# Kernel tuning notes

Measured on AMD Instinct MI355X. Metric: run time of the kernel, lower is better.

## Reference

```python
import jax, jax.numpy as jnp
import numpy as np

ALPHA = (0.02, 0.04, 0.08, 0.16)
CHAMFER_W, SMOOTH_W, CURVATURE_W = 1.0, 1.0, 0.3
NS = (8192, 4096, 2048, 1024)
B = 2


def _sqdist(a, b):
    # a: [B,N,3], b: [B,M,3] -> [B,N,M] squared euclidean distance
    return (jnp.sum(a * a, axis=-1)[:, :, None]
            - 2.0 * jnp.einsum('bnc,bmc->bnm', a, b)
            + jnp.sum(b * b, axis=-1)[:, None, :])


def _knn(d, k):
    # k smallest distances + indices along last axis
    neg, idx = jax.lax.top_k(-d, k)
    return -neg, idx


def _gather(points, idx):
    # points: [B,M,C], idx: [B,N,K] -> [B,N,K,C]
    return jax.vmap(lambda p, i: p[i])(points, idx)


def _scale_loss(pc1, pc2, flow):
    # pc1, pc2, flow: [B,3,N]-like -> permute to points-last layout
    p1 = jnp.transpose(pc1, (0, 2, 1))   # [B,N,3]
    p2 = jnp.transpose(pc2, (0, 2, 1))   # [B,M,3]
    fl = jnp.transpose(flow, (0, 2, 1))  # [B,N,3]
    warp = p1 + fl                        # warped pc1

    # curvature of pc2 (10-NN on pc2 itself)
    _, k22 = _knn(_sqdist(p2, p2), 10)
    cv2 = jnp.sum(_gather(p2, k22) - p2[:, :, None, :], axis=2) / 9.0  # [B,M,3]

    # 10-NN on pc1 (shared for warped curvature and smoothness; 9-NN is prefix)
    _, k11 = _knn(_sqdist(p1, p1), 10)
    cvw = jnp.sum(_gather(warp, k11) - warp[:, :, None, :], axis=2) / 9.0  # [B,N,3]

    k9 = k11[:, :, :9]
    gfl = _gather(fl, k9)  # [B,N,9,3]
    smooth = jnp.sum(jnp.linalg.norm(gfl - fl[:, :, None, :], axis=3), axis=2) / 8.0  # [B,N]

    # chamfer between warped pc1 and pc2
    d12 = _sqdist(warp, p2)               # [B,N,M]
    dist1 = jnp.min(d12, axis=-1)         # [B,N]
    dist2 = jnp.min(d12, axis=1)          # [B,M]

    # inverse-distance interpolation of pc2 curvature onto warped pc1 (5-NN)
    dist, kidx = _knn(d12, 5)             # [B,N,5]
    gcv = _gather(cv2, kidx)              # [B,N,5,3]
    w = 1.0 / (dist + 1e-8)
    w = w / jnp.sum(w, axis=2, keepdims=True)
    inter = jnp.sum(w[..., None] * gcv, axis=2)  # [B,N,3]

    chamfer = jnp.mean(jnp.sum(dist1, axis=1)) + jnp.mean(jnp.sum(dist2, axis=1))
    smoothness = jnp.mean(jnp.sum(smooth, axis=1))
    curv = jnp.mean(jnp.sum(jnp.sum((inter - cvw) ** 2, axis=2), axis=1))
    return chamfer, smoothness, curv


def setup_inputs() -> dict:
    key = jax.random.key(0)
    keys = jax.random.split(key, 12)
    out = {}
    names = ['pc1', 'pc2', 'flow']
    k = 0
    for name in names:
        for i, n in enumerate(NS):
            scale = 1.0 if name != 'flow' else 0.1
            out[f'{name}_{i}'] = scale * jax.random.normal(keys[k], (B, 3, n), dtype=jnp.float32)
            k += 1
    return out


def reference(pc1_0, pc1_1, pc1_2, pc1_3,
              pc2_0, pc2_1, pc2_2, pc2_3,
              flow_0, flow_1, flow_2, flow_3):
    pcs1 = (pc1_0, pc1_1, pc1_2, pc1_3)
    pcs2 = (pc2_0, pc2_1, pc2_2, pc2_3)
    flows = (flow_0, flow_1, flow_2, flow_3)
    ch = sm = cv = jnp.float32(0.0)
    for a, p1, p2, fl in zip(ALPHA, pcs1, pcs2, flows):
        c, s, k = _scale_loss(p1, p2, fl)
        ch = ch + a * c
        sm = sm + a * s
        cv = cv + a * k
    total = CHAMFER_W * ch + CURVATURE_W * cv + SMOOTH_W * sm
    return jnp.reshape(total, (1,))
```

## Files before the change

### kernel.cpp

```cpp
#include <hip/hip_runtime.h>
#include <math.h>


#define BLOCK 512
#define UNIT 1024
#define NTOT 15360
#define MASKC 0xFFFFE000u
#define PB 340

typedef unsigned int uint;

struct Params {
  const float* pc1[4];
  const float* pc2[4];
  const float* fl[4];
  float4* cv2;
  float4* cvw;
  float* out;
};

__device__ __forceinline__ void decode(int r, int wv, int& s, int& b,
                                       int& i0, int& lo, int& N, int& cpw,
                                       int& off, float& alpha) {
  int rr;
  if (r < 256)      { s = 0; rr = r; }
  else if (r < 320) { s = 1; rr = r - 256; }
  else if (r < 336) { s = 2; rr = r - 320; }
  else              { s = 3; rr = r - 336; }
  N = 8192 >> s;
  cpw = 8 >> s;
  int perb = 128 >> (2 * s);
  b = rr >> (7 - 2 * s);
  int chunk = rr & (perb - 1);
  int qg = (chunk << s) + (wv >> (3 - s));
  i0 = qg << 6;
  lo = (wv & (cpw - 1)) << 10;
  off = 16384 - (16384 >> s);
  alpha = 0.02f * (float)(1 << s);
}

__device__ __forceinline__ float wave_sum(float v) {
  #pragma unroll
  for (int o = 32; o; o >>= 1) v += __shfl_down(v, o, 64);
  return v;
}

template <int K>
__device__ __forceinline__ void key_insert(float (&kd)[K], float kf) {
  #pragma unroll
  for (int m = K - 1; m >= 1; --m)
    kd[m] = __builtin_amdgcn_fmed3f(kf, kd[m - 1], kd[m]);
  kd[0] = fminf(kd[0], kf);
}

template <int K>
__device__ __forceinline__ void merge_pair(float (&a)[K], const float (&b)[K]) {
  #pragma unroll
  for (int m = 0; m < K; ++m) key_insert<K>(a, b[m]);
}

__device__ __forceinline__ float pack_key(float d, float iw) {
  return __uint_as_float((__float_as_uint(d) & MASKC) | __float_as_uint(iw));
}

template <int K, bool WARP, bool PACK>
__device__ void scan_u(const float* px, const float* py, const float* pz,
                       const float* fx, const float* fy, const float* fz,
                       int lo, float ax, float ay, float az,
                       float (&a)[K], float (&b)[K], float4* tile,
                       int lane) {
  int j = lo + lane;
  float x = px[j], y = py[j], z = pz[j];
  if (WARP) { x += fx[j]; y += fy[j]; z += fz[j]; }
  for (int c0 = lo; c0 < lo + UNIT; c0 += 64) {
    tile[lane] = make_float4(x, y, z, __uint_as_float((uint)(c0 + lane)));
    asm volatile("s_waitcnt lgkmcnt(0)" ::: "memory");
    if (c0 + 64 < lo + UNIT) {
      int jn = j + 64;
      x = px[jn]; y = py[jn]; z = pz[jn];
      if (WARP) { x += fx[jn]; y += fy[jn]; z += fz[jn]; }
    }
    #pragma unroll 8
    for (int t = 0; t < 64; t += 2) {
      float4 cA = tile[t];
      float4 cB = tile[t + 1];
      float dxa = ax - cA.x, dya = ay - cA.y, dza = az - cA.z;
      float dA = fmaf(dxa, dxa, fmaf(dya, dya, dza * dza));
      float dxb = ax - cB.x, dyb = ay - cB.y, dzb = az - cB.z;
      float dB = fmaf(dxb, dxb, fmaf(dyb, dyb, dzb * dzb));
      if (PACK) {
        key_insert<K>(a, pack_key(dA, cA.w));
        key_insert<K>(b, pack_key(dB, cB.w));
      } else {
        a[0] = fminf(a[0], dA);
        b[0] = fminf(b[0], dB);
      }
    }
    j += 64;
  }
}

template <int K>
__device__ __forceinline__ bool merge_group(float (&a)[K], float* sm,
                                            int tid, int cpw) {
  const int STR = K | 1;
  int q = tid & 63, wv = tid >> 6;
  #pragma unroll
  for (int m = 0; m < K; ++m) sm[(wv * 64 + q) * STR + m] = a[m];
  __syncthreads();
  if (wv & (cpw - 1)) return false;
  for (int w = wv + 1; w < wv + cpw; ++w)
    #pragma unroll
    for (int m = 0; m < K; ++m)
      key_insert<K>(a, sm[(w * 64 + q) * STR + m]);
  return true;
}

__global__ __launch_bounds__(1) void k_zero(float* out) { out[0] = 0.f; }

__global__ __launch_bounds__(BLOCK, 8) void k_fused(Params P) {
  __shared__ float4 tiles[8][64];
  __shared__ float sm[8 * 64 * 11];
  int tid = threadIdx.x, q = tid & 63, wv = tid >> 6;
  int pass = blockIdx.x / PB, r = blockIdx.x % PB;
  int s, b, i0, lo, N, cpw, off; float alpha;
  decode(r, wv, s, b, i0, lo, N, cpw, off, alpha);
  int i = i0 + q;
  float4* tile = tiles[wv];

  if (pass == 0) {
    const float* p2 = P.pc2[s] + b * 3 * N;
    float ax = p2[i], ay = p2[N + i], az = p2[2 * N + i];
    float a[10], bb[10];
    #pragma unroll
    for (int m = 0; m < 10; ++m) { a[m] = 3.0e38f; bb[m] = 3.0e38f; }
    scan_u<10, false, true>(p2, p2 + N, p2 + 2 * N, nullptr, nullptr,
                            nullptr, lo, ax, ay, az, a, bb, tile, q);
    merge_pair<10>(a, bb);
    if (!merge_group<10>(a, sm, tid, cpw)) return;
    float sx = 0.f, sy = 0.f, sz = 0.f;
    #pragma unroll
    for (int m = 0; m < 10; ++m) {
      int j = (int)(__float_as_uint(a[m]) & 0x1FFFu);
      sx += p2[j]; sy += p2[N + j]; sz += p2[2 * N + j];
    }
    const float inv9 = 1.f / 9.f;
    P.cv2[b * NTOT + off + i] = make_float4((sx - 10.f * ax) * inv9,
                                            (sy - 10.f * ay) * inv9,
                                            (sz - 10.f * az) * inv9, 0.f);
  } else if (pass == 1) {
    const float* p1 = P.pc1[s] + b * 3 * N;
    const float* fl = P.fl[s] + b * 3 * N;
    float ax = p1[i], ay = p1[N + i], az = p1[2 * N + i];
    float a[10], bb[10];
    #pragma unroll
    for (int m = 0; m < 10; ++m) { a[m] = 3.0e38f; bb[m] = 3.0e38f; }
    scan_u<10, false, true>(p1, p1 + N, p1 + 2 * N, nullptr, nullptr,
                            nullptr, lo, ax, ay, az, a, bb, tile, q);
    merge_pair<10>(a, bb);
    if (!merge_group<10>(a, sm, tid, cpw)) return;
    float fix = fl[i], fiy = fl[N + i], fiz = fl[2 * N + i];
    float wix = ax + fix, wiy = ay + fiy, wiz = az + fiz;
    float sx = 0.f, sy = 0.f, sz = 0.f, smooth = 0.f;
    float dmax = -1.f, worst = 0.f;
    #pragma unroll
    for (int m = 0; m < 10; ++m) {
      int j = (int)(__float_as_uint(a[m]) & 0x1FFFu);
      float px = p1[j], py = p1[N + j], pz = p1[2 * N + j];
      float flx = fl[j], fly = fl[N + j], flz = fl[2 * N + j];
      sx += px + flx; sy += py + fly; sz += pz + flz;
      float ddx = px - ax, ddy = py - ay, ddz = pz - az;
      float d = fmaf(ddx, ddx, fmaf(ddy, ddy, ddz * ddz));
      float gx = flx - fix, gy = fly - fiy, gz = flz - fiz;
      float term = sqrtf(fmaf(gx, gx, fmaf(gy, gy, gz * gz)));
      smooth += term;
      if (d > dmax) { dmax = d; worst = term; }
    }
    smooth -= worst;
    const float inv9 = 1.f / 9.f;
    P.cvw[b * NTOT + off + i] = make_float4((sx - 10.f * wix) * inv9,
                                            (sy - 10.f * wiy) * inv9,
                                            (sz - 10.f * wiz) * inv9, 0.f);
    float ssum = wave_sum(smooth * (1.f / 8.f));
    if (q == 0) atomicAdd(P.out, alpha * 0.5f * ssum);
  } else {
    const float* p1 = P.pc1[s] + b * 3 * N;
    const float* fl = P.fl[s] + b * 3 * N;
    const float* p2 = P.pc2[s] + b * 3 * N;
    float ax = p2[i], ay = p2[N + i], az = p2[2 * N + i];
    float a[1], bb[1];
    a[0] = 3.0e38f; bb[0] = 3.0e38f;
    scan_u<1, true, false>(p1, p1 + N, p1 + 2 * N, fl, fl + N, fl + 2 * N,
                           lo, ax, ay, az, a, bb, tile, q);
    merge_pair<1>(a, bb);
    if (!merge_group<1>(a, sm, tid, cpw)) return;
    float msum = wave_sum(a[0]);
    if (q == 0) atomicAdd(P.out, alpha * 0.5f * msum);
  }
}

__global__ __launch_bounds__(BLOCK, 8) void k_cross(Params P) {
  __shared__ float4 tiles[8][64];
  __shared__ float sm[8 * 64 * 5];
  int tid = threadIdx.x, q = tid & 63, wv = tid >> 6;
  int s, b, i0, lo, N, cpw, off; float alpha;
  decode(blockIdx.x, wv, s, b, i0, lo, N, cpw, off, alpha);
  int i = i0 + q;
  const float* p1 = P.pc1[s] + b * 3 * N;
  const float* fl = P.fl[s] + b * 3 * N;
  const float* p2 = P.pc2[s] + b * 3 * N;
  float ax = p1[i] + fl[i], ay = p1[N + i] + fl[N + i],
        az = p1[2 * N + i] + fl[2 * N + i];
  float a[5], bb[5];
  #pragma unroll
  for (int m = 0; m < 5; ++m) { a[m] = 3.0e38f; bb[m] = 3.0e38f; }
  scan_u<5, false, true>(p2, p2 + N, p2 + 2 * N, nullptr, nullptr, nullptr,
                         lo, ax, ay, az, a, bb, tiles[wv], q);
  merge_pair<5>(a, bb);
  if (!merge_group<5>(a, sm, tid, cpw)) return;
  float dist1 = 3.0e38f, wsum = 0.f, ix = 0.f, iy = 0.f, iz = 0.f;
  #pragma unroll
  for (int m = 0; m < 5; ++m) {
    int j = (int)(__float_as_uint(a[m]) & 0x1FFFu);
    float px = p2[j], py = p2[N + j], pz = p2[2 * N + j];
    float ddx = px - ax, ddy = py - ay, ddz = pz - az;
    float d = fmaf(ddx, ddx, fmaf(ddy, ddy, ddz * ddz));
    dist1 = fminf(dist1, d);
    float w = 1.f / (d + 1e-8f);
    wsum += w;
    float4 cv = P.cv2[b * NTOT + off + j];
    ix += w * cv.x; iy += w * cv.y; iz += w * cv.z;
  }
  float inv = 1.f / wsum;
  ix *= inv; iy *= inv; iz *= inv;
  float4 cw = P.cvw[b * NTOT + off + i];
  float ex = ix - cw.x, ey = iy - cw.y, ez = iz - cw.z;
  float curv = fmaf(ex, ex, fmaf(ey, ey, ez * ez));
  float csum = wave_sum(dist1 + 0.3f * curv);
  if (q == 0) atomicAdd(P.out, alpha * 0.5f * csum);
}

extern "C" void kernel_launch(void* const* d_in, const int* in_sizes, int n_in,
                              void* d_out, int out_size, void* d_ws,
                              size_t ws_size, hipStream_t stream) {
  Params P;
  for (int s = 0; s < 4; ++s) {
    P.pc1[s] = (const float*)d_in[s];
    P.pc2[s] = (const float*)d_in[4 + s];
    P.fl[s]  = (const float*)d_in[8 + s];
  }
  P.cv2 = (float4*)d_ws;
  P.cvw = (float4*)((char*)d_ws + (size_t)2 * NTOT * sizeof(float4));
  P.out = (float*)d_out;

  k_zero<<<dim3(1), dim3(1), 0, stream>>>(P.out);
  k_fused<<<dim3(3 * PB), dim3(BLOCK), 0, stream>>>(P);
  k_cross<<<dim3(PB), dim3(BLOCK), 0, stream>>>(P);
}
```

Before: 326.9 us.

## Move cross kNN scan into fused kernel and add lightweight tail kernel

The warped-pc1 to pc2 5-NN scan moves out of the separate cross kernel and becomes a fourth pass inside the fused kernel. It writes packed keys to workspace, and a small tail kernel then computes interpolation, curvature and dist1. Block-to-pass mapping is interleaved (blockIdx & 3) so heavy scans from different passes mix across CUs, and the dependency on cv2/cvw is moved to the cheap tail. The aim is to remove the serialized second heavy launch and its tail imbalance, at the cost of an extra workspace round-trip for the keys.

```diff
diff --git a/kernel.cpp b/kernel.cpp
--- a/kernel.cpp
+++ b/kernel.cpp
@@ -7,6 +7,7 @@
 #define NTOT 15360
 #define MASKC 0xFFFFE000u
 #define PB 340
+#define STR 11
 
 typedef unsigned int uint;
 
@@ -16,6 +17,7 @@
   const float* fl[4];
   float4* cv2;
   float4* cvw;
+  float* ckeys;
   float* out;
 };
 
@@ -103,7 +105,6 @@
 template <int K>
 __device__ __forceinline__ bool merge_group(float (&a)[K], float* sm,
                                             int tid, int cpw) {
-  const int STR = K | 1;
   int q = tid & 63, wv = tid >> 6;
   #pragma unroll
   for (int m = 0; m < K; ++m) sm[(wv * 64 + q) * STR + m] = a[m];
@@ -120,16 +121,19 @@
 
 __global__ __launch_bounds__(BLOCK, 8) void k_fused(Params P) {
   __shared__ float4 tiles[8][64];
-  __shared__ float sm[8 * 64 * 11];
+  __shared__ float sm[8 * 64 * STR];
   int tid = threadIdx.x, q = tid & 63, wv = tid >> 6;
-  int pass = blockIdx.x / PB, r = blockIdx.x % PB;
+  int pass = blockIdx.x & 3, r = blockIdx.x >> 2;
   int s, b, i0, lo, N, cpw, off; float alpha;
   decode(r, wv, s, b, i0, lo, N, cpw, off, alpha);
   int i = i0 + q;
   float4* tile = tiles[wv];
 
+  const float* p1 = P.pc1[s] + b * 3 * N;
+  const float* fl = P.fl[s] + b * 3 * N;
+  const float* p2 = P.pc2[s] + b * 3 * N;
+
   if (pass == 0) {
-    const float* p2 = P.pc2[s] + b * 3 * N;
     float ax = p2[i], ay = p2[N + i], az = p2[2 * N + i];
     float a[10], bb[10];
     #pragma unroll
@@ -149,8 +153,6 @@
                                             (sy - 10.f * ay) * inv9,
                                             (sz - 10.f * az) * inv9, 0.f);
   } else if (pass == 1) {
-    const float* p1 = P.pc1[s] + b * 3 * N;
-    const float* fl = P.fl[s] + b * 3 * N;
     float ax = p1[i], ay = p1[N + i], az = p1[2 * N + i];
     float a[10], bb[10];
     #pragma unroll
@@ -183,10 +185,20 @@
                                             (sz - 10.f * wiz) * inv9, 0.f);
     float ssum = wave_sum(smooth * (1.f / 8.f));
     if (q == 0) atomicAdd(P.out, alpha * 0.5f * ssum);
+  } else if (pass == 2) {
+    float ax = p1[i] + fl[i], ay = p1[N + i] + fl[N + i],
+          az = p1[2 * N + i] + fl[2 * N + i];
+    float a[5], bb[5];
+    #pragma unroll
+    for (int m = 0; m < 5; ++m) { a[m] = 3.0e38f; bb[m] = 3.0e38f; }
+    scan_u<5, false, true>(p2, p2 + N, p2 + 2 * N, nullptr, nullptr,
+                           nullptr, lo, ax, ay, az, a, bb, tile, q);
+    merge_pair<5>(a, bb);
+    if (!merge_group<5>(a, sm, tid, cpw)) return;
+    #pragma unroll
+    for (int m = 0; m < 5; ++m)
+      P.ckeys[(b * NTOT + off + i) * 5 + m] = a[m];
   } else {
-    const float* p1 = P.pc1[s] + b * 3 * N;
-    const float* fl = P.fl[s] + b * 3 * N;
-    const float* p2 = P.pc2[s] + b * 3 * N;
     float ax = p2[i], ay = p2[N + i], az = p2[2 * N + i];
     float a[1], bb[1];
     a[0] = 3.0e38f; bb[0] = 3.0e38f;
@@ -199,29 +211,25 @@
   }
 }
 
-__global__ __launch_bounds__(BLOCK, 8) void k_cross(Params P) {
-  __shared__ float4 tiles[8][64];
-  __shared__ float sm[8 * 64 * 5];
-  int tid = threadIdx.x, q = tid & 63, wv = tid >> 6;
-  int s, b, i0, lo, N, cpw, off; float alpha;
-  decode(blockIdx.x, wv, s, b, i0, lo, N, cpw, off, alpha);
-  int i = i0 + q;
+__global__ __launch_bounds__(256) void k_tail(Params P) {
+  int g = blockIdx.x * 256 + threadIdx.x;
+  int b = (g >= NTOT) ? 1 : 0;
+  int t = g - b * NTOT;
+  int s = (t < 8192) ? 0 : (t < 12288) ? 1 : (t < 14336) ? 2 : 3;
+  int off = 16384 - (16384 >> s);
+  int N = 8192 >> s;
+  int i = t - off;
+  float alpha = 0.02f * (float)(1 << s);
   const float* p1 = P.pc1[s] + b * 3 * N;
   const float* fl = P.fl[s] + b * 3 * N;
   const float* p2 = P.pc2[s] + b * 3 * N;
   float ax = p1[i] + fl[i], ay = p1[N + i] + fl[N + i],
         az = p1[2 * N + i] + fl[2 * N + i];
-  float a[5], bb[5];
-  #pragma unroll
-  for (int m = 0; m < 5; ++m) { a[m] = 3.0e38f; bb[m] = 3.0e38f; }
-  scan_u<5, false, true>(p2, p2 + N, p2 + 2 * N, nullptr, nullptr, nullptr,
-                         lo, ax, ay, az, a, bb, tiles[wv], q);
-  merge_pair<5>(a, bb);
-  if (!merge_group<5>(a, sm, tid, cpw)) return;
   float dist1 = 3.0e38f, wsum = 0.f, ix = 0.f, iy = 0.f, iz = 0.f;
   #pragma unroll
   for (int m = 0; m < 5; ++m) {
-    int j = (int)(__float_as_uint(a[m]) & 0x1FFFu);
+    float key = P.ckeys[(b * NTOT + t) * 5 + m];
+    int j = (int)(__float_as_uint(key) & 0x1FFFu);
     float px = p2[j], py = p2[N + j], pz = p2[2 * N + j];
     float ddx = px - ax, ddy = py - ay, ddz = pz - az;
     float d = fmaf(ddx, ddx, fmaf(ddy, ddy, ddz * ddz));
@@ -233,11 +241,12 @@
   }
   float inv = 1.f / wsum;
   ix *= inv; iy *= inv; iz *= inv;
-  float4 cw = P.cvw[b * NTOT + off + i];
+  float4 cw = P.cvw[b * NTOT + t];
   float ex = ix - cw.x, ey = iy - cw.y, ez = iz - cw.z;
   float curv = fmaf(ex, ex, fmaf(ey, ey, ez * ez));
-  float csum = wave_sum(dist1 + 0.3f * curv);
-  if (q == 0) atomicAdd(P.out, alpha * 0.5f * csum);
+  float v = alpha * (dist1 + 0.3f * curv);
+  float csum = wave_sum(v);
+  if ((threadIdx.x & 63) == 0) atomicAdd(P.out, 0.5f * csum);
 }
 
 extern "C" void kernel_launch(void* const* d_in, const int* in_sizes, int n_in,
@@ -250,10 +259,11 @@
     P.fl[s]  = (const float*)d_in[8 + s];
   }
   P.cv2 = (float4*)d_ws;
-  P.cvw = (float4*)((char*)d_ws + (size_t)2 * NTOT * sizeof(float4));
+  P.cvw = P.cv2 + 2 * NTOT;
+  P.ckeys = (float*)(P.cvw + 2 * NTOT);
   P.out = (float*)d_out;
 
   k_zero<<<dim3(1), dim3(1), 0, stream>>>(P.out);
-  k_fused<<<dim3(3 * PB), dim3(BLOCK), 0, stream>>>(P);
-  k_cross<<<dim3(PB), dim3(BLOCK), 0, stream>>>(P);
-}
+  k_fused<<<dim3(4 * PB), dim3(BLOCK), 0, stream>>>(P);
+  k_tail<<<dim3(120), dim3(256), 0, stream>>>(P);
+}
```

Result: slower. 392.8 us (+20.1%).
